# Kernel optimization log

Measured on AMD Instinct MI355X. Metric: run time of the kernel, lower is better.

## Reference

```python
import jax, jax.numpy as jnp
import numpy as np

N_NODES = 50000
N_EDGES = 800000
NEG_SLOPE = 0.2  # PyG GATConv default


def _glorot(key, shape):
    fan_in = shape[0] if len(shape) > 1 else shape[0]
    return jax.random.normal(key, shape, dtype=jnp.float32) / jnp.sqrt(jnp.float32(fan_in))


def setup_inputs() -> dict:
    key = jax.random.key(0)
    ks = jax.random.split(key, 12)
    x = jax.random.normal(ks[0], (N_NODES, 128), dtype=jnp.float32)
    edge_index = jax.random.randint(ks[1], (2, N_EDGES), 0, N_NODES, dtype=jnp.int64)
    return {
        "x": x,
        "edge_index": edge_index,
        # GAT layer 1: 128 -> 128 (heads=1)
        "W1": _glorot(ks[2], (128, 128)),
        "a_src1": _glorot(ks[3], (128,)),
        "a_dst1": _glorot(ks[4], (128,)),
        "b1": jnp.zeros((128,), dtype=jnp.float32),
        "Wres1": _glorot(ks[5], (128, 128)),
        # GAT layer 2: 128 -> 256
        "W2": _glorot(ks[6], (128, 256)),
        "a_src2": _glorot(ks[7], (256,)),
        "a_dst2": _glorot(ks[8], (256,)),
        "b2": jnp.zeros((256,), dtype=jnp.float32),
        "Wres2": _glorot(ks[9], (128, 256)),
    }


def _gat_layer(x, src, dst, W, a_src, a_dst, b, Wres, n):
    # h: [N, C_out] transformed node features
    h = x @ W
    # per-edge attention logit: gather scalar contributions, LeakyReLU
    logit = jax.nn.leaky_relu((h @ a_src)[src] + (h @ a_dst)[dst], NEG_SLOPE)  # [E]
    # numerically stable segment softmax over incoming edges of each dst node
    seg_max = jax.ops.segment_max(logit, dst, num_segments=n)  # [N]
    ex = jnp.exp(logit - seg_max[dst])
    denom = jax.ops.segment_sum(ex, dst, num_segments=n)  # [N]
    alpha = ex / denom[dst]  # [E]; self-loops guarantee denom > 0
    # weighted scatter-add aggregation
    out = jax.ops.segment_sum(alpha[:, None] * h[src], dst, num_segments=n)  # [N, C_out]
    # residual projection (in_dim != out_dim) + bias
    return out + x @ Wres + b


def reference(x, edge_index, W1, a_src1, a_dst1, b1, Wres1, W2, a_src2, a_dst2, b2, Wres2):
    n = x.shape[0]
    loops = jnp.arange(n, dtype=edge_index.dtype)  # add_self_loops=True (PyG default)
    src = jnp.concatenate([edge_index[0], loops])
    dst = jnp.concatenate([edge_index[1], loops])
    h = _gat_layer(x, src, dst, W1, a_src1, a_dst1, b1, Wres1, n)
    h = jax.nn.relu(h)
    return _gat_layer(h, src, dst, W2, a_src2, a_dst2, b2, Wres2, n)
```

## Files before the change

kernel.cpp:

```cpp
#include <hip/hip_runtime.h>
#include <math.h>

typedef __attribute__((ext_vector_type(8))) short bf16x8;
typedef __attribute__((ext_vector_type(4))) float f32x4;

__device__ inline unsigned short f2bf(float f) {
  union { float f; unsigned u; } x; x.f = f;
  unsigned r = x.u + 0x7FFF + ((x.u >> 16) & 1);
  return (unsigned short)(r >> 16);
}
__device__ inline float bf2f(unsigned short b) {
  union { unsigned u; float f; } x; x.u = ((unsigned)b) << 16;
  return x.f;
}


__global__ void convert_kernel(const void* edges, int E, int N,
                               int* __restrict__ src32, int* __restrict__ dst32,
                               int* __restrict__ counts) {
  int i = blockIdx.x * blockDim.x + threadIdx.x;
  int tot = E + N;
  if (i >= tot) return;
  int s, d;
  if (i < E) {
    const long long* q = (const long long*)edges;
    bool i64 = true;
#pragma unroll
    for (int k = 0; k < 8; ++k) {
      long long v = q[k];
      if (v < 0 || v >= (long long)N) i64 = false;
    }
    if (i64) {
      s = (int)q[i];
      d = (int)q[E + i];
    } else {
      s = ((const int*)edges)[i];
      d = ((const int*)edges)[E + i];
    }
  } else {
    s = d = i - E;
  }
  src32[i] = s;
  dst32[i] = d;
  atomicAdd(&counts[d], 1);
}


__global__ __launch_bounds__(256) void scan_partial(const int* __restrict__ counts,
                                                    int* __restrict__ bsum, int n) {
  int t = threadIdx.x;
  int base = blockIdx.x * 1024 + t * 4;
  int s = 0;
#pragma unroll
  for (int k = 0; k < 4; ++k) {
    int i = base + k;
    if (i < n) s += counts[i];
  }
#pragma unroll
  for (int off = 32; off; off >>= 1) s += __shfl_xor(s, off);
  __shared__ int red[4];
  if ((t & 63) == 0) red[t >> 6] = s;
  __syncthreads();
  if (t == 0) bsum[blockIdx.x] = red[0] + red[1] + red[2] + red[3];
}

__global__ __launch_bounds__(256) void scan_bsum(const int* __restrict__ bsum,
                                                 int* __restrict__ ebsum,
                                                 int* __restrict__ rowptr, int nblk, int n) {
  __shared__ int sh[256];
  int t = threadIdx.x;
  int v = (t < nblk) ? bsum[t] : 0;
  sh[t] = v;
  __syncthreads();
  for (int off = 1; off < 256; off <<= 1) {
    int u = (t >= off) ? sh[t - off] : 0;
    __syncthreads();
    sh[t] += u;
    __syncthreads();
  }
  if (t < nblk) ebsum[t] = sh[t] - v;
  if (t == nblk - 1) rowptr[n] = sh[t];
}

__global__ __launch_bounds__(256) void scan_final(const int* __restrict__ counts,
                                                  const int* __restrict__ ebsum,
                                                  int* __restrict__ rowptr,
                                                  int* __restrict__ cursor, int n) {
  int t = threadIdx.x;
  int lane = t & 63;
  int wv = t >> 6;
  int base = blockIdx.x * 1024 + t * 4;
  int c[4];
  int ts = 0;
#pragma unroll
  for (int k = 0; k < 4; ++k) {
    int i = base + k;
    c[k] = (i < n) ? counts[i] : 0;
    ts += c[k];
  }
  int ws = ts;
  for (int off = 1; off < 64; off <<= 1) {
    int u = __shfl_up(ws, off);
    if (lane >= off) ws += u;
  }
  __shared__ int wtot[4];
  if (lane == 63) wtot[wv] = ws;
  __syncthreads();
  int woff = 0;
  for (int k = 0; k < 4; ++k)
    if (k < wv) woff += wtot[k];
  int run = ebsum[blockIdx.x] + woff + (ws - ts);
#pragma unroll
  for (int k = 0; k < 4; ++k) {
    int i = base + k;
    if (i < n) {
      rowptr[i] = run;
      cursor[i] = run;
    }
    run += c[k];
  }
}

__global__ void scatter_kernel(const int* __restrict__ src32, const int* __restrict__ dst32,
                               int* __restrict__ cursor, int* __restrict__ csr_src, int tot) {
  int i = blockIdx.x * blockDim.x + threadIdx.x;
  if (i >= tot) return;
  int d = dst32[i];
  int slot = atomicAdd(&cursor[d], 1);
  csr_src[slot] = src32[i];
}


__global__ void cvt_all(const float* __restrict__ x,
                        const float* __restrict__ W1, const float* __restrict__ Wres1,
                        const float* __restrict__ W2, const float* __restrict__ Wres2,
                        unsigned short* __restrict__ x16,
                        unsigned short* __restrict__ w1t, unsigned short* __restrict__ wres1t,
                        unsigned short* __restrict__ w2t, unsigned short* __restrict__ wres2t,
                        int N, int Mpad) {
  int tid = blockIdx.x * blockDim.x + threadIdx.x;
  int xcnt = Mpad * 32;
  if (tid < xcnt) {
    int row = tid >> 5;
    int q = (tid & 31) << 2;
    unsigned short o0 = 0, o1 = 0, o2 = 0, o3 = 0;
    if (row < N) {
      float4 v = *(const float4*)(x + (size_t)row * 128 + q);
      o0 = f2bf(v.x); o1 = f2bf(v.y); o2 = f2bf(v.z); o3 = f2bf(v.w);
    }
    unsigned short* p = x16 + (size_t)row * 128 + q;
    p[0] = o0; p[1] = o1; p[2] = o2; p[3] = o3;
    return;
  }
  int t2 = tid - xcnt;
  const float* W;
  unsigned short* Wt;
  int C, loc;
  if (t2 < 16384) { W = W1; Wt = w1t; C = 128; loc = t2; }
  else if (t2 < 32768) { W = Wres1; Wt = wres1t; C = 128; loc = t2 - 16384; }
  else if (t2 < 65536) { W = W2; Wt = w2t; C = 256; loc = t2 - 32768; }
  else if (t2 < 98304) { W = Wres2; Wt = wres2t; C = 256; loc = t2 - 65536; }
  else return;
  int c = loc >> 7;
  int k = loc & 127;
  Wt[(size_t)c * 128 + k] = f2bf(W[(size_t)k * C + c]);
}


template <int MODE>
__global__ __launch_bounds__(256) void gemm_mfma(const unsigned short* __restrict__ A,
                                                 const unsigned short* __restrict__ Bt,
                                                 unsigned short* __restrict__ Cout,
                                                 const float* __restrict__ bias,
                                                 int Nrows, int Ctot) {
  int l = threadIdx.x & 63;
  int w = threadIdx.x >> 6;
  int row_w = blockIdx.x * 128 + (w & 1) * 64;
  int col_w = blockIdx.y * 128 + (w >> 1) * 64;
  int lo = l & 15, hi = l >> 4;
  f32x4 acc[4][4];
#pragma unroll
  for (int i = 0; i < 4; ++i)
#pragma unroll
    for (int j = 0; j < 4; ++j) acc[i][j] = (f32x4){0.f, 0.f, 0.f, 0.f};

  const unsigned short* Ap = A + (size_t)(row_w + lo) * 128 + hi * 8;
  const unsigned short* Bp = Bt + (size_t)(col_w + lo) * 128 + hi * 8;
#pragma unroll
  for (int kk = 0; kk < 4; ++kk) {
    bf16x8 a[4], b[4];
#pragma unroll
    for (int f = 0; f < 4; ++f) {
      a[f] = *(const bf16x8*)(Ap + (size_t)f * 16 * 128 + kk * 32);
      b[f] = *(const bf16x8*)(Bp + (size_t)f * 16 * 128 + kk * 32);
    }
#pragma unroll
    for (int fr = 0; fr < 4; ++fr)
#pragma unroll
      for (int fc = 0; fc < 4; ++fc)
        acc[fr][fc] = __builtin_amdgcn_mfma_f32_16x16x32_bf16(a[fr], b[fc], acc[fr][fc], 0, 0, 0);
  }
#pragma unroll
  for (int fr = 0; fr < 4; ++fr) {
#pragma unroll
    for (int r = 0; r < 4; ++r) {
      int row = row_w + fr * 16 + hi * 4 + r;
      if (row < Nrows) {
#pragma unroll
        for (int fc = 0; fc < 4; ++fc) {
          int col = col_w + fc * 16 + lo;
          float v = acc[fr][fc][r];
          if (MODE == 1) v += bias[col];
          Cout[(size_t)row * Ctot + col] = f2bf(v);
        }
      }
    }
  }
}


template <int C>
__global__ void scalars_kernel(const unsigned short* __restrict__ h,
                               const float* __restrict__ a_src,
                               const float* __restrict__ a_dst, float* __restrict__ as_,
                               float* __restrict__ ad_, int N) {
  int wid = (blockIdx.x * blockDim.x + threadIdx.x) >> 6;
  int lane = threadIdx.x & 63;
  if (wid >= N) return;
  const int FPL = C / 64;
  const unsigned short* hr = h + (size_t)wid * C + FPL * lane;
  float s1 = 0.f, s2 = 0.f;
#pragma unroll
  for (int j = 0; j < FPL; ++j) {
    float v = bf2f(hr[j]);
    s1 += v * a_src[FPL * lane + j];
    s2 += v * a_dst[FPL * lane + j];
  }
#pragma unroll
  for (int off = 32; off; off >>= 1) {
    s1 += __shfl_xor(s1, off);
    s2 += __shfl_xor(s2, off);
  }
  if (lane == 0) {
    as_[wid] = s1;
    ad_[wid] = s2;
  }
}


template <int C, bool L1>
__global__ __launch_bounds__(256) void aggregate_kernel(
    const unsigned short* __restrict__ h, unsigned short* __restrict__ res,
    float* __restrict__ outf,
    const float* __restrict__ as_, const float* __restrict__ ad_,
    const int* __restrict__ rowptr, const int* __restrict__ csr_src, int N) {
  const int FPL = C / 64;
  int wid = blockIdx.x * 4 + (threadIdx.x >> 6);
  int lane = threadIdx.x & 63;
  if (wid >= N) return;
  int base = rowptr[wid];
  int deg = rowptr[wid + 1] - base;
  float adn = ad_[wid];
  float m = -1e30f, ssum = 0.f;
  float acc[FPL];
#pragma unroll
  for (int c = 0; c < FPL; ++c) acc[c] = 0.f;
  for (int b0 = 0; b0 < deg; b0 += 64) {
    int idx = b0 + lane;
    int s = 0;
    float logit = -1e30f;
    if (idx < deg) {
      s = csr_src[base + idx];
      float tt = as_[s] + adn;
      logit = tt > 0.f ? tt : 0.2f * tt;
    }
    float cm = logit;
#pragma unroll
    for (int off = 32; off; off >>= 1) cm = fmaxf(cm, __shfl_xor(cm, off));
    float mnew = fmaxf(m, cm);
    float scale = __expf(m - mnew);
    ssum *= scale;
#pragma unroll
    for (int c = 0; c < FPL; ++c) acc[c] *= scale;
    float p = (idx < deg) ? __expf(logit - mnew) : 0.f;
    float ps = p;
#pragma unroll
    for (int off = 32; off; off >>= 1) ps += __shfl_xor(ps, off);
    ssum += ps;
    int cnt = min(64, deg - b0);
    int j = 0;
    for (; j + 4 <= cnt; j += 4) {
      float pj0 = __shfl(p, j), pj1 = __shfl(p, j + 1);
      float pj2 = __shfl(p, j + 2), pj3 = __shfl(p, j + 3);
      int sj0 = __shfl(s, j), sj1 = __shfl(s, j + 1);
      int sj2 = __shfl(s, j + 2), sj3 = __shfl(s, j + 3);
      const unsigned short* h0 = h + (size_t)sj0 * C + FPL * lane;
      const unsigned short* h1 = h + (size_t)sj1 * C + FPL * lane;
      const unsigned short* h2 = h + (size_t)sj2 * C + FPL * lane;
      const unsigned short* h3 = h + (size_t)sj3 * C + FPL * lane;
      if (FPL == 2) {
        ushort2 v0 = *(const ushort2*)h0, v1 = *(const ushort2*)h1;
        ushort2 v2 = *(const ushort2*)h2, v3 = *(const ushort2*)h3;
        acc[0] = fmaf(pj0, bf2f(v0.x), acc[0]); acc[1] = fmaf(pj0, bf2f(v0.y), acc[1]);
        acc[0] = fmaf(pj1, bf2f(v1.x), acc[0]); acc[1] = fmaf(pj1, bf2f(v1.y), acc[1]);
        acc[0] = fmaf(pj2, bf2f(v2.x), acc[0]); acc[1] = fmaf(pj2, bf2f(v2.y), acc[1]);
        acc[0] = fmaf(pj3, bf2f(v3.x), acc[0]); acc[1] = fmaf(pj3, bf2f(v3.y), acc[1]);
      } else {
        ushort4 v0 = *(const ushort4*)h0, v1 = *(const ushort4*)h1;
        ushort4 v2 = *(const ushort4*)h2, v3 = *(const ushort4*)h3;
        acc[0] = fmaf(pj0, bf2f(v0.x), acc[0]); acc[1] = fmaf(pj0, bf2f(v0.y), acc[1]);
        acc[2] = fmaf(pj0, bf2f(v0.z), acc[2]); acc[3] = fmaf(pj0, bf2f(v0.w), acc[3]);
        acc[0] = fmaf(pj1, bf2f(v1.x), acc[0]); acc[1] = fmaf(pj1, bf2f(v1.y), acc[1]);
        acc[2] = fmaf(pj1, bf2f(v1.z), acc[2]); acc[3] = fmaf(pj1, bf2f(v1.w), acc[3]);
        acc[0] = fmaf(pj2, bf2f(v2.x), acc[0]); acc[1] = fmaf(pj2, bf2f(v2.y), acc[1]);
        acc[2] = fmaf(pj2, bf2f(v2.z), acc[2]); acc[3] = fmaf(pj2, bf2f(v2.w), acc[3]);
        acc[0] = fmaf(pj3, bf2f(v3.x), acc[0]); acc[1] = fmaf(pj3, bf2f(v3.y), acc[1]);
        acc[2] = fmaf(pj3, bf2f(v3.z), acc[2]); acc[3] = fmaf(pj3, bf2f(v3.w), acc[3]);
      }
    }
    for (; j < cnt; ++j) {
      float pj = __shfl(p, j);
      int sj = __shfl(s, j);
      const unsigned short* hs = h + (size_t)sj * C + FPL * lane;
      if (FPL == 2) {
        ushort2 hv = *(const ushort2*)hs;
        acc[0] = fmaf(pj, bf2f(hv.x), acc[0]);
        acc[1] = fmaf(pj, bf2f(hv.y), acc[1]);
      } else {
        ushort4 hv = *(const ushort4*)hs;
        acc[0] = fmaf(pj, bf2f(hv.x), acc[0]);
        acc[1] = fmaf(pj, bf2f(hv.y), acc[1]);
        acc[2] = fmaf(pj, bf2f(hv.z), acc[2]);
        acc[3] = fmaf(pj, bf2f(hv.w), acc[3]);
      }
    }
    m = mnew;
  }
  float inv = 1.f / ssum;
  size_t o = (size_t)wid * C + FPL * lane;
  if (L1) {
    unsigned short* p = res + o;
    ushort2 rv = *(const ushort2*)p;
    float v0 = fmaxf(acc[0] * inv + bf2f(rv.x), 0.f);
    float v1 = fmaxf(acc[1] * inv + bf2f(rv.y), 0.f);
    ushort2 ov; ov.x = f2bf(v0); ov.y = f2bf(v1);
    *(ushort2*)p = ov;
  } else {
    ushort4 rv = *(const ushort4*)(res + o);
    float4 ov;
    ov.x = acc[0] * inv + bf2f(rv.x);
    ov.y = acc[1] * inv + bf2f(rv.y);
    ov.z = acc[2] * inv + bf2f(rv.z);
    ov.w = acc[3] * inv + bf2f(rv.w);
    *(float4*)(outf + o) = ov;
  }
}


extern "C" void kernel_launch(void* const* d_in, const int* in_sizes, int n_in,
                              void* d_out, int out_size, void* d_ws, size_t ws_size,
                              hipStream_t stream) {
  const float* x = (const float*)d_in[0];
  const void* edges = d_in[1];
  const float* W1 = (const float*)d_in[2];
  const float* a_src1 = (const float*)d_in[3];
  const float* a_dst1 = (const float*)d_in[4];
  const float* b1 = (const float*)d_in[5];
  const float* Wres1 = (const float*)d_in[6];
  const float* W2 = (const float*)d_in[7];
  const float* a_src2 = (const float*)d_in[8];
  const float* a_dst2 = (const float*)d_in[9];
  const float* b2 = (const float*)d_in[10];
  const float* Wres2 = (const float*)d_in[11];
  float* out = (float*)d_out;

  int N = in_sizes[0] / 128;
  int E = in_sizes[1] / 2;
  int TOT = E + N;
  int Mpad = (N + 127) & ~127;
  int nblk = (N + 1023) >> 10;

  char* w = (char*)d_ws;
  size_t off = 0;
  auto alloc = [&](size_t bytes) {
    char* p = w + off;
    off += (bytes + 255) & ~(size_t)255;
    return p;
  };
  int* counts = (int*)alloc((size_t)N * 4);
  int* cursor = (int*)alloc((size_t)N * 4);
  int* rowptr = (int*)alloc((size_t)(N + 1) * 4);
  int* bsum = (int*)alloc(1024);
  int* ebsum = (int*)alloc(1024);
  float* as_ = (float*)alloc((size_t)N * 4);
  float* ad_ = (float*)alloc((size_t)N * 4);
  int* src32 = (int*)alloc((size_t)TOT * 4);
  int* dst32 = (int*)alloc((size_t)TOT * 4);
  int* csr = (int*)alloc((size_t)TOT * 4);
  unsigned short* x16 = (unsigned short*)alloc((size_t)Mpad * 128 * 2);
  unsigned short* w1t = (unsigned short*)alloc(128 * 128 * 2);
  unsigned short* wres1t = (unsigned short*)alloc(128 * 128 * 2);
  unsigned short* w2t = (unsigned short*)alloc(256 * 128 * 2);
  unsigned short* wres2t = (unsigned short*)alloc(256 * 128 * 2);
  unsigned short* h16 = (unsigned short*)alloc((size_t)N * 256 * 2);
  unsigned short* out1 = (unsigned short*)alloc((size_t)Mpad * 128 * 2);
  unsigned short* res2 = (unsigned short*)alloc((size_t)Mpad * 256 * 2);

  hipMemsetAsync(counts, 0, (size_t)N * 4, stream);
  hipMemsetAsync(out1 + (size_t)N * 128, 0, (size_t)(Mpad - N) * 128 * 2, stream);

  int gb = (TOT + 255) / 256;
  convert_kernel<<<gb, 256, 0, stream>>>(edges, E, N, src32, dst32, counts);
  scan_partial<<<nblk, 256, 0, stream>>>(counts, bsum, N);
  scan_bsum<<<1, 256, 0, stream>>>(bsum, ebsum, rowptr, nblk, N);
  scan_final<<<nblk, 256, 0, stream>>>(counts, ebsum, rowptr, cursor, N);
  scatter_kernel<<<gb, 256, 0, stream>>>(src32, dst32, cursor, csr, TOT);

  cvt_all<<<(Mpad * 32 + 98304 + 255) / 256, 256, 0, stream>>>(
      x, W1, Wres1, W2, Wres2, x16, w1t, wres1t, w2t, wres2t, N, Mpad);

  int mt = Mpad / 128;
  int sb = (N + 3) / 4;

  gemm_mfma<0><<<dim3(mt, 1), 256, 0, stream>>>(x16, w1t, h16, nullptr, N, 128);
  gemm_mfma<1><<<dim3(mt, 1), 256, 0, stream>>>(x16, wres1t, out1, b1, N, 128);
  scalars_kernel<128><<<sb, 256, 0, stream>>>(h16, a_src1, a_dst1, as_, ad_, N);
  aggregate_kernel<128, true><<<sb, 256, 0, stream>>>(h16, out1, nullptr, as_, ad_, rowptr, csr, N);

  gemm_mfma<0><<<dim3(mt, 2), 256, 0, stream>>>(out1, w2t, h16, nullptr, N, 256);
  gemm_mfma<1><<<dim3(mt, 2), 256, 0, stream>>>(out1, wres2t, res2, b2, N, 256);
  scalars_kernel<256><<<sb, 256, 0, stream>>>(h16, a_src2, a_dst2, as_, ad_, N);
  aggregate_kernel<256, false><<<sb, 256, 0, stream>>>(h16, res2, out, as_, ad_, rowptr, csr, N);
}
```

Before: 387.9 us.

## Fuse dual GEMMs with attention scalar computation and widen aggregation unroll

Merges the feature and residual GEMMs into one kernel that shares the A-tile loads, and computes the per-node attention dot products in its epilogue with shuffles and atomics. This removes the separate scalars kernel and one launch per layer. It also widens the gather loop in aggregation from 4 to 8 edges so more loads are in flight. In exchange it doubles accumulator registers in the GEMM, which may lower occupancy, adds memsets and atomics, and computes the scalars from fp32 values instead of bf16-rounded ones.

```diff
diff --git a/kernel.cpp b/kernel.cpp
--- a/kernel.cpp
+++ b/kernel.cpp
@@ -167,38 +167,55 @@
 }
 
 
-template <int MODE>
-__global__ __launch_bounds__(256) void gemm_mfma(const unsigned short* __restrict__ A,
-                                                 const unsigned short* __restrict__ Bt,
-                                                 unsigned short* __restrict__ Cout,
-                                                 const float* __restrict__ bias,
-                                                 int Nrows, int Ctot) {
+__global__ __launch_bounds__(256) void gemm_dual(
+    const unsigned short* __restrict__ A,
+    const unsigned short* __restrict__ Bh, const unsigned short* __restrict__ Br,
+    unsigned short* __restrict__ Hout, unsigned short* __restrict__ Rout,
+    const float* __restrict__ bias,
+    const float* __restrict__ a_src, const float* __restrict__ a_dst,
+    float* __restrict__ as_, float* __restrict__ ad_,
+    int Nrows, int Ctot) {
   int l = threadIdx.x & 63;
   int w = threadIdx.x >> 6;
   int row_w = blockIdx.x * 128 + (w & 1) * 64;
   int col_w = blockIdx.y * 128 + (w >> 1) * 64;
   int lo = l & 15, hi = l >> 4;
-  f32x4 acc[4][4];
+  f32x4 ah[4][4], ar[4][4];
 #pragma unroll
   for (int i = 0; i < 4; ++i)
 #pragma unroll
-    for (int j = 0; j < 4; ++j) acc[i][j] = (f32x4){0.f, 0.f, 0.f, 0.f};
+    for (int j = 0; j < 4; ++j) {
+      ah[i][j] = (f32x4){0.f, 0.f, 0.f, 0.f};
+      ar[i][j] = (f32x4){0.f, 0.f, 0.f, 0.f};
+    }
 
   const unsigned short* Ap = A + (size_t)(row_w + lo) * 128 + hi * 8;
-  const unsigned short* Bp = Bt + (size_t)(col_w + lo) * 128 + hi * 8;
+  const unsigned short* Bhp = Bh + (size_t)(col_w + lo) * 128 + hi * 8;
+  const unsigned short* Brp = Br + (size_t)(col_w + lo) * 128 + hi * 8;
 #pragma unroll
   for (int kk = 0; kk < 4; ++kk) {
-    bf16x8 a[4], b[4];
+    bf16x8 a[4], bh[4], br[4];
 #pragma unroll
     for (int f = 0; f < 4; ++f) {
       a[f] = *(const bf16x8*)(Ap + (size_t)f * 16 * 128 + kk * 32);
-      b[f] = *(const bf16x8*)(Bp + (size_t)f * 16 * 128 + kk * 32);
+      bh[f] = *(const bf16x8*)(Bhp + (size_t)f * 16 * 128 + kk * 32);
+      br[f] = *(const bf16x8*)(Brp + (size_t)f * 16 * 128 + kk * 32);
     }
 #pragma unroll
     for (int fr = 0; fr < 4; ++fr)
 #pragma unroll
-      for (int fc = 0; fc < 4; ++fc)
-        acc[fr][fc] = __builtin_amdgcn_mfma_f32_16x16x32_bf16(a[fr], b[fc], acc[fr][fc], 0, 0, 0);
+      for (int fc = 0; fc < 4; ++fc) {
+        ah[fr][fc] = __builtin_amdgcn_mfma_f32_16x16x32_bf16(a[fr], bh[fc], ah[fr][fc], 0, 0, 0);
+        ar[fr][fc] = __builtin_amdgcn_mfma_f32_16x16x32_bf16(a[fr], br[fc], ar[fr][fc], 0, 0, 0);
+      }
+  }
+  float wsrc[4], wdst[4], wb[4];
+#pragma unroll
+  for (int fc = 0; fc < 4; ++fc) {
+    int col = col_w + fc * 16 + lo;
+    wsrc[fc] = a_src[col];
+    wdst[fc] = a_dst[col];
+    wb[fc] = bias[col];
   }
 #pragma unroll
   for (int fr = 0; fr < 4; ++fr) {
@@ -206,44 +223,27 @@
     for (int r = 0; r < 4; ++r) {
       int row = row_w + fr * 16 + hi * 4 + r;
       if (row < Nrows) {
+        float s1 = 0.f, s2 = 0.f;
 #pragma unroll
         for (int fc = 0; fc < 4; ++fc) {
           int col = col_w + fc * 16 + lo;
-          float v = acc[fr][fc][r];
-          if (MODE == 1) v += bias[col];
-          Cout[(size_t)row * Ctot + col] = f2bf(v);
+          float vh = ah[fr][fc][r];
+          Hout[(size_t)row * Ctot + col] = f2bf(vh);
+          s1 = fmaf(vh, wsrc[fc], s1);
+          s2 = fmaf(vh, wdst[fc], s2);
+          Rout[(size_t)row * Ctot + col] = f2bf(ar[fr][fc][r] + wb[fc]);
+        }
+#pragma unroll
+        for (int off = 8; off; off >>= 1) {
+          s1 += __shfl_xor(s1, off);
+          s2 += __shfl_xor(s2, off);
+        }
+        if (lo == 0) {
+          atomicAdd(&as_[row], s1);
+          atomicAdd(&ad_[row], s2);
         }
       }
     }
-  }
-}
-
-
-template <int C>
-__global__ void scalars_kernel(const unsigned short* __restrict__ h,
-                               const float* __restrict__ a_src,
-                               const float* __restrict__ a_dst, float* __restrict__ as_,
-                               float* __restrict__ ad_, int N) {
-  int wid = (blockIdx.x * blockDim.x + threadIdx.x) >> 6;
-  int lane = threadIdx.x & 63;
-  if (wid >= N) return;
-  const int FPL = C / 64;
-  const unsigned short* hr = h + (size_t)wid * C + FPL * lane;
-  float s1 = 0.f, s2 = 0.f;
-#pragma unroll
-  for (int j = 0; j < FPL; ++j) {
-    float v = bf2f(hr[j]);
-    s1 += v * a_src[FPL * lane + j];
-    s2 += v * a_dst[FPL * lane + j];
-  }
-#pragma unroll
-  for (int off = 32; off; off >>= 1) {
-    s1 += __shfl_xor(s1, off);
-    s2 += __shfl_xor(s2, off);
-  }
-  if (lane == 0) {
-    as_[wid] = s1;
-    ad_[wid] = s2;
   }
 }
 
@@ -289,33 +289,36 @@
     ssum += ps;
     int cnt = min(64, deg - b0);
     int j = 0;
-    for (; j + 4 <= cnt; j += 4) {
-      float pj0 = __shfl(p, j), pj1 = __shfl(p, j + 1);
-      float pj2 = __shfl(p, j + 2), pj3 = __shfl(p, j + 3);
-      int sj0 = __shfl(s, j), sj1 = __shfl(s, j + 1);
-      int sj2 = __shfl(s, j + 2), sj3 = __shfl(s, j + 3);
-      const unsigned short* h0 = h + (size_t)sj0 * C + FPL * lane;
-      const unsigned short* h1 = h + (size_t)sj1 * C + FPL * lane;
-      const unsigned short* h2 = h + (size_t)sj2 * C + FPL * lane;
-      const unsigned short* h3 = h + (size_t)sj3 * C + FPL * lane;
+    for (; j + 8 <= cnt; j += 8) {
+      float pj[8];
+      int sj[8];
+#pragma unroll
+      for (int u = 0; u < 8; ++u) {
+        pj[u] = __shfl(p, j + u);
+        sj[u] = __shfl(s, j + u);
+      }
       if (FPL == 2) {
-        ushort2 v0 = *(const ushort2*)h0, v1 = *(const ushort2*)h1;
-        ushort2 v2 = *(const ushort2*)h2, v3 = *(const ushort2*)h3;
-        acc[0] = fmaf(pj0, bf2f(v0.x), acc[0]); acc[1] = fmaf(pj0, bf2f(v0.y), acc[1]);
-        acc[0] = fmaf(pj1, bf2f(v1.x), acc[0]); acc[1] = fmaf(pj1, bf2f(v1.y), acc[1]);
-        acc[0] = fmaf(pj2, bf2f(v2.x), acc[0]); acc[1] = fmaf(pj2, bf2f(v2.y), acc[1]);
-        acc[0] = fmaf(pj3, bf2f(v3.x), acc[0]); acc[1] = fmaf(pj3, bf2f(v3.y), acc[1]);
+        ushort2 v[8];
+#pragma unroll
+        for (int u = 0; u < 8; ++u)
+          v[u] = *(const ushort2*)(h + (size_t)sj[u] * C + FPL * lane);
+#pragma unroll
+        for (int u = 0; u < 8; ++u) {
+          acc[0] = fmaf(pj[u], bf2f(v[u].x), acc[0]);
+          acc[1] = fmaf(pj[u], bf2f(v[u].y), acc[1]);
+        }
       } else {
-        ushort4 v0 = *(const ushort4*)h0, v1 = *(const ushort4*)h1;
-        ushort4 v2 = *(const ushort4*)h2, v3 = *(const ushort4*)h3;
-        acc[0] = fmaf(pj0, bf2f(v0.x), acc[0]); acc[1] = fmaf(pj0, bf2f(v0.y), acc[1]);
-        acc[2] = fmaf(pj0, bf2f(v0.z), acc[2]); acc[3] = fmaf(pj0, bf2f(v0.w), acc[3]);
-        acc[0] = fmaf(pj1, bf2f(v1.x), acc[0]); acc[1] = fmaf(pj1, bf2f(v1.y), acc[1]);
-        acc[2] = fmaf(pj1, bf2f(v1.z), acc[2]); acc[3] = fmaf(pj1, bf2f(v1.w), acc[3]);
-        acc[0] = fmaf(pj2, bf2f(v2.x), acc[0]); acc[1] = fmaf(pj2, bf2f(v2.y), acc[1]);
-        acc[2] = fmaf(pj2, bf2f(v2.z), acc[2]); acc[3] = fmaf(pj2, bf2f(v2.w), acc[3]);
-        acc[0] = fmaf(pj3, bf2f(v3.x), acc[0]); acc[1] = fmaf(pj3, bf2f(v3.y), acc[1]);
-        acc[2] = fmaf(pj3, bf2f(v3.z), acc[2]); acc[3] = fmaf(pj3, bf2f(v3.w), acc[3]);
+        ushort4 v[8];
+#pragma unroll
+        for (int u = 0; u < 8; ++u)
+          v[u] = *(const ushort4*)(h + (size_t)sj[u] * C + FPL * lane);
+#pragma unroll
+        for (int u = 0; u < 8; ++u) {
+          acc[0] = fmaf(pj[u], bf2f(v[u].x), acc[0]);
+          acc[1] = fmaf(pj[u], bf2f(v[u].y), acc[1]);
+          acc[2] = fmaf(pj[u], bf2f(v[u].z), acc[2]);
+          acc[3] = fmaf(pj[u], bf2f(v[u].w), acc[3]);
+        }
       }
     }
     for (; j < cnt; ++j) {
@@ -422,13 +425,15 @@
   int mt = Mpad / 128;
   int sb = (N + 3) / 4;
 
-  gemm_mfma<0><<<dim3(mt, 1), 256, 0, stream>>>(x16, w1t, h16, nullptr, N, 128);
-  gemm_mfma<1><<<dim3(mt, 1), 256, 0, stream>>>(x16, wres1t, out1, b1, N, 128);
-  scalars_kernel<128><<<sb, 256, 0, stream>>>(h16, a_src1, a_dst1, as_, ad_, N);
+  hipMemsetAsync(as_, 0, (size_t)N * 4, stream);
+  hipMemsetAsync(ad_, 0, (size_t)N * 4, stream);
+  gemm_dual<<<dim3(mt, 1), 256, 0, stream>>>(x16, w1t, wres1t, h16, out1, b1,
+                                             a_src1, a_dst1, as_, ad_, N, 128);
   aggregate_kernel<128, true><<<sb, 256, 0, stream>>>(h16, out1, nullptr, as_, ad_, rowptr, csr, N);
 
-  gemm_mfma<0><<<dim3(mt, 2), 256, 0, stream>>>(out1, w2t, h16, nullptr, N, 256);
-  gemm_mfma<1><<<dim3(mt, 2), 256, 0, stream>>>(out1, wres2t, res2, b2, N, 256);
-  scalars_kernel<256><<<sb, 256, 0, stream>>>(h16, a_src2, a_dst2, as_, ad_, N);
+  hipMemsetAsync(as_, 0, (size_t)N * 4, stream);
+  hipMemsetAsync(ad_, 0, (size_t)N * 4, stream);
+  gemm_dual<<<dim3(mt, 2), 256, 0, stream>>>(out1, w2t, wres2t, h16, res2, b2,
+                                             a_src2, a_dst2, as_, ad_, N, 256);
   aggregate_kernel<256, false><<<sb, 256, 0, stream>>>(h16, res2, out, as_, ad_, rowptr, csr, N);
 }
```

After: 398.4 us. 2.7% more time.
